# Kernel tuning notes

Measured on AMD Instinct MI355X. Metric: run time of the kernel, lower is better.

Reference implementation:

```python
import jax, jax.numpy as jnp
import numpy as np

B, SECL, WORDL = 16, 8, 512
S = SECL * WORDL
H, E, V, NOOV = 256, 128, 50000, 32
EOS = 3
FSIZE = 2  # config.mode == 'train'


def setup_inputs() -> dict:
    key = jax.random.key(0)
    ks = jax.random.split(key, 24)
    g = lambda i, shape, s=0.02: jax.random.normal(ks[i], shape, jnp.float32) * s
    inp = jax.random.randint(ks[0], (B,), 0, V)
    inp = inp.at[:4].set(EOS)  # exercise focus-update branch
    h = g(1, (B, H), 0.1)
    c = g(2, (B, H), 0.1)
    enc_outputs = g(3, (B, S, 2 * H), 1.0)
    enc_feature = g(4, (B, S, 2 * H), 0.1)
    enc_sec_output = g(5, (B, SECL, 2 * H), 1.0)
    enc_mask = jnp.ones((B, S), jnp.float32)
    sec_mask = jnp.ones((B, SECL), jnp.float32)
    prev_context = g(6, (B, 2 * H), 0.1)
    zeros_oov = jnp.zeros((B, NOOV), jnp.float32)
    enc_input_oov = jax.random.randint(ks[7], (B, S), 0, V + NOOV)
    coverage = jnp.zeros((B, S), jnp.float32)
    # sparse nonneg focus distribution over sections (guaranteed >=1 nonzero/row)
    u = jax.random.uniform(ks[8], (B, SECL))
    f = u * (u > 0.5)
    fb = jax.nn.one_hot(jnp.argmax(u, axis=1), SECL)
    f = jnp.where(f.sum(1, keepdims=True) > 0, f, fb)
    focus = f / f.sum(1, keepdims=True)
    params = dict(
        embedding=g(9, (V, E)),
        W_comb=g(10, (E, 2 * H + E)), b_comb=jnp.zeros((E,), jnp.float32),
        W_ih=g(11, (4 * H, E)), W_hh=g(12, (4 * H, H)),
        b_ih=jnp.zeros((4 * H,), jnp.float32), b_hh=jnp.zeros((4 * H,), jnp.float32),
        W_d=g(13, (2 * H, 2 * H)), b_d=jnp.zeros((2 * H,), jnp.float32),
        W_feat=g(14, (2 * H, 2 * H)), v_sec=g(15, (2 * H,)),
        W_dec=g(16, (2 * H, 2 * H)), b_dec=jnp.zeros((2 * H,), jnp.float32),
        w_cov=g(17, (2 * H,)), v_att=g(18, (2 * H,)),
        W_pgen=g(19, (1, 4 * H + E)), b_pgen=jnp.zeros((1,), jnp.float32),
        W_out=g(20, (V, 3 * H)), b_out=g(21, (V,)),
    )
    return dict(inp=inp, h=h, c=c, enc_outputs=enc_outputs, enc_feature=enc_feature,
                enc_sec_output=enc_sec_output, enc_mask=enc_mask, sec_mask=sec_mask,
                prev_context=prev_context, zeros_oov=zeros_oov, enc_input_oov=enc_input_oov,
                coverage=coverage, focus=focus, **params)


def _focus_update(focus, sad):
    # rem_mask: positions from the first nonzero of focus onward
    fz = jnp.cumprod((focus == 0).astype(sad.dtype), axis=1)
    rem_mask = (fz == 0).astype(sad.dtype)
    focus_index = jnp.sum(fz, axis=1).astype(jnp.int32)  # index of first nonzero
    focus_mask = jax.nn.one_hot(focus_index, SECL, dtype=sad.dtype)
    rem_ex = rem_mask - focus_mask
    focus_beta = sad * focus_mask
    rem_beta = sad * rem_ex
    max_rem_beta = rem_beta.max(axis=1)
    max_rem_ind = jnp.argmax(rem_beta, axis=1)
    compare = (focus_beta.max(axis=1) * 2 > max_rem_beta).astype(sad.dtype)[:, None]
    # train branch
    src = (max_rem_beta != 0).astype(sad.dtype)[:, None]
    max_rem_mask = jax.nn.one_hot(max_rem_ind, SECL, dtype=sad.dtype) * src
    cp2 = jnp.cumprod((max_rem_mask == 0).astype(sad.dtype), axis=1)
    after = (cp2 == 0).astype(sad.dtype) - max_rem_mask
    amb = sad * after
    mam_mask = (jax.nn.one_hot(jnp.argmax(amb, axis=1), SECL, dtype=sad.dtype)
                * (amb.max(axis=1) != 0).astype(sad.dtype)[:, None])
    case_f = focus_beta + sad * max_rem_mask
    case_r = sad * (max_rem_mask + mam_mask)
    fu = compare * case_f + (1 - compare) * case_r
    return fu / fu.sum(1, keepdims=True)


def reference(inp, h, c, enc_outputs, enc_feature, enc_sec_output, enc_mask, sec_mask,
              prev_context, zeros_oov, enc_input_oov, coverage, focus,
              embedding, W_comb, b_comb, W_ih, W_hh, b_ih, b_hh,
              W_d, b_d, W_feat, v_sec, W_dec, b_dec, w_cov, v_att,
              W_pgen, b_pgen, W_out, b_out):
    inp_is_eos = (inp == EOS).astype(jnp.float32)[:, None]  # [B,1] -> bcast over secL
    emb = embedding[inp]  # [B,E]
    x = jnp.concatenate([prev_context, emb], axis=1) @ W_comb.T + b_comb  # [B,E]
    # single LSTM step (torch gate order i,f,g,o)
    gates = x @ W_ih.T + b_ih + h @ W_hh.T + b_hh
    gi_, gf_, gg_, go_ = jnp.split(gates, 4, axis=1)
    c_new = jax.nn.sigmoid(gf_) * c + jax.nn.sigmoid(gi_) * jnp.tanh(gg_)
    h_new = jax.nn.sigmoid(go_) * jnp.tanh(c_new)
    dec_state = jnp.concatenate([h_new, c_new], axis=1)  # [B,2H]
    # section attention
    feat = enc_sec_output @ W_feat.T  # [B,secL,2H]
    d = dec_state @ W_d.T + b_d
    sc = jnp.tanh(feat + d[:, None, :]) @ v_sec  # [B,secL]
    sad = jax.nn.softmax(sc, axis=1) * sec_mask
    sad = sad / sad.sum(1, keepdims=True)
    # hard-attention focus update (only where input was EOS)
    fu = _focus_update(focus, sad)
    focus = inp_is_eos * fu + (1 - inp_is_eos) * focus
    # word attention with coverage
    dfeat = dec_state @ W_dec.T + b_dec
    att = enc_feature + dfeat[:, None, :] + coverage[:, :, None] * w_cov[None, None, :]
    score = jnp.tanh(att) @ v_att  # [B,S]
    score3 = score.reshape(B, SECL, WORDL)
    topk_focus, gidx = jax.lax.top_k(focus, FSIZE)  # [B,FSIZE]
    bidx = jnp.arange(B)[:, None]
    score_g = score3[bidx, gidx].reshape(B, FSIZE * WORDL)
    mask_g = enc_mask.reshape(B, SECL, WORDL)[bidx, gidx].reshape(B, FSIZE * WORDL)
    af = jax.nn.softmax(score_g, axis=1) * mask_g
    af = af / af.sum(1, keepdims=True)
    af = topk_focus[:, :, None] * af.reshape(B, FSIZE, WORDL)
    attn = jnp.zeros((B, SECL, WORDL), af.dtype).at[bidx, gidx].set(af).reshape(B, S)
    attn = attn / attn.sum(1, keepdims=True)
    context = jnp.einsum('bs,bsd->bd', attn, enc_outputs)  # [B,2H]
    coverage = coverage + attn
    # pointer-generator
    p_gen = jax.nn.sigmoid(jnp.concatenate([context, dec_state, x], axis=1) @ W_pgen.T + b_pgen)
    logits = jnp.concatenate([h_new, context], axis=1) @ W_out.T + b_out
    vocab_dist = jax.nn.softmax(logits, axis=1)
    vext = jnp.concatenate([p_gen * vocab_dist, zeros_oov], axis=1)  # [B,V+NOOV]
    final = vext.at[bidx, enc_input_oov].add((1 - p_gen) * attn)
    return final, h_new, c_new, context, attn, coverage, focus, sad
```

## Files before the change

kernel.cpp:

```cpp
#include <hip/hip_runtime.h>
#include <math.h>

#define NB 16
#define SECL 8
#define WORDL 512
#define SS 4096
#define HH 256
#define EE 128
#define VV 50000
#define NOOV 32
#define VO 50032
#define EOS_ID 3
#define H2 512
#define KOUT 768

#define OFF_FINAL 0
#define OFF_H    800512
#define OFF_C    804608
#define OFF_CTX  808704
#define OFF_ATTN 816896
#define OFF_COV  882432
#define OFF_FOC  947968
#define OFF_SAD  948096

#define WX     0
#define WD     2048
#define WDF    10240
#define WSC    18432
#define WGI    18560
#define WTF    18592
#define WSG    18624
#define WPART  35008
#define WPG    166080
#define WLG    166512

__device__ __forceinline__ float sigm(float x){ return 1.f/(1.f+__expf(-x)); }
__device__ __forceinline__ float tfast(float x){
  float ax = fabsf(x);
  float e  = __expf(-2.f*ax);
  float t  = (1.f-e)/(1.f+e);
  return x < 0.f ? -t : t;
}
__device__ __forceinline__ float dot4(float acc, float4 a, float4 b){
  acc = fmaf(a.x,b.x,acc); acc = fmaf(a.y,b.y,acc);
  acc = fmaf(a.z,b.z,acc); acc = fmaf(a.w,b.w,acc);
  return acc;
}
__device__ __forceinline__ float dot2(float acc, float2 a, float2 b){
  acc = fmaf(a.x,b.x,acc); acc = fmaf(a.y,b.y,acc);
  return acc;
}
__device__ __forceinline__ float mergep(float a, float b, int k, int lane){
  float send = (lane & k) ? a : b;
  float recv = __shfl_xor(send, k);
  return (lane & k) ? b + recv : a + recv;
}
__device__ __forceinline__ float reduce8(float acc[8], int lane){
  float m0 = mergep(acc[0], acc[1], 1, lane);
  float m1 = mergep(acc[2], acc[3], 1, lane);
  float m2 = mergep(acc[4], acc[5], 1, lane);
  float m3 = mergep(acc[6], acc[7], 1, lane);
  float n0 = mergep(m0, m1, 2, lane);
  float n1 = mergep(m2, m3, 2, lane);
  float p  = mergep(n0, n1, 4, lane);
  p += __shfl_xor(p, 8);
  p += __shfl_xor(p, 16);
  p += __shfl_xor(p, 32);
  return p;
}

__device__ __forceinline__ void focus_compute(int b, const float sc[SECL],
    const int* inp, const float* smask, const float* focus_in,
    float fo[SECL], float sad[SECL], int* pi1, int* pi2, float* pv1, float* pv2){
  float f[SECL];
  float mx = -1e30f;
  for(int l=0;l<SECL;l++) mx = fmaxf(mx, sc[l]);
  float sum = 0.f;
  for(int l=0;l<SECL;l++){ sad[l] = __expf(sc[l]-mx); sum += sad[l]; }
  float s2 = 0.f;
  for(int l=0;l<SECL;l++){ sad[l] = sad[l]/sum * smask[b*SECL+l]; s2 += sad[l]; }
  for(int l=0;l<SECL;l++) sad[l] /= s2;
  for(int l=0;l<SECL;l++) f[l] = focus_in[b*SECL+l];
  int fi = SECL;
  for(int l=0;l<SECL;l++){ if(f[l] != 0.f){ fi = l; break; } }
  float rem[SECL];
  for(int l=0;l<SECL;l++) rem[l] = (l > fi) ? sad[l] : 0.f;
  float mrb = rem[0]; int mri = 0;
  for(int l=1;l<SECL;l++){ if(rem[l] > mrb){ mrb = rem[l]; mri = l; } }
  float fbm = (fi < SECL) ? sad[fi] : 0.f;
  int cmp = (fbm*2.f > mrb);
  int src = (mrb != 0.f);
  float amb[SECL];
  for(int l=0;l<SECL;l++) amb[l] = (src && l > mri) ? sad[l] : 0.f;
  float am = amb[0]; int ai = 0;
  for(int l=1;l<SECL;l++){ if(amb[l] > am){ am = amb[l]; ai = l; } }
  float fu[SECL]; float fs = 0.f;
  for(int l=0;l<SECL;l++){
    float mrm = (src && l == mri) ? 1.f : 0.f;
    float mam = ((am != 0.f) && l == ai) ? 1.f : 0.f;
    float cf = ((l==fi) ? sad[l] : 0.f) + sad[l]*mrm;
    float cr = sad[l]*(mrm + mam);
    fu[l] = cmp ? cf : cr;
    fs += fu[l];
  }
  float eos = (inp[b] == EOS_ID) ? 1.f : 0.f;
  for(int l=0;l<SECL;l++)
    fo[l] = eos*(fu[l]/fs) + (1.f-eos)*f[l];
  float v1 = fo[0]; int i1 = 0;
  for(int l=1;l<SECL;l++){ if(fo[l] > v1){ v1 = fo[l]; i1 = l; } }
  float v2 = -1e30f; int i2 = 0;
  for(int l=0;l<SECL;l++){ if(l != i1 && fo[l] > v2){ v2 = fo[l]; i2 = l; } }
  *pi1 = i1; *pi2 = i2; *pv1 = v1; *pv2 = v2;
}


__global__ void __launch_bounds__(256)
k_x(const int* __restrict__ inp, const float* __restrict__ pc,
    const float* __restrict__ emb, const float* __restrict__ Wc,
    const float* __restrict__ bc, float* __restrict__ ws){
  int lane = threadIdx.x & 63;
  int gw = blockIdx.x*4 + (threadIdx.x >> 6);
  int bg = gw & 1, e = gw >> 1;
  float4 z = {0,0,0,0};
  float4 i0[8], i1[8], i2[8];
  #pragma unroll
  for(int j=0;j<8;j++){
    int b = bg*8 + j;
    i0[j] = *(const float4*)(pc + b*H2 + lane*4);
    i1[j] = *(const float4*)(pc + b*H2 + 256 + lane*4);
    i2[j] = (lane < 32) ? *(const float4*)(emb + (size_t)inp[b]*EE + lane*4) : z;
  }
  const float* wr = Wc + (size_t)e*(H2+EE);
  float4 w0 = *(const float4*)(wr + lane*4);
  float4 w1 = *(const float4*)(wr + 256 + lane*4);
  float4 w2 = (lane < 32) ? *(const float4*)(wr + 512 + lane*4) : z;
  float acc[8];
  #pragma unroll
  for(int j=0;j<8;j++){
    float a = dot4(0.f, w0, i0[j]);
    a = dot4(a, w1, i1[j]);
    a = dot4(a, w2, i2[j]);
    acc[j] = a;
  }
  float p = reduce8(acc, lane);
  if(lane < 8) ws[WX + (bg*8+lane)*EE + e] = p + bc[e];
}

__global__ void __launch_bounds__(256)
k_gates(const float* __restrict__ h, const float* __restrict__ c,
        const float* __restrict__ Wih, const float* __restrict__ Whh,
        const float* __restrict__ bih, const float* __restrict__ bhh,
        const float* __restrict__ ws, float* __restrict__ out){
  __shared__ float g_lds[4][8];
  int lane = threadIdx.x & 63;
  int wv   = threadIdx.x >> 6;
  int j  = blockIdx.x >> 1;
  int bg = blockIdx.x & 1;
  float2 xb[8]; float4 hb[8];
  #pragma unroll
  for(int q=0;q<8;q++){
    int b = bg*8 + q;
    xb[q] = *(const float2*)(ws + WX + b*EE + lane*2);
    hb[q] = *(const float4*)(h + b*HH + lane*4);
  }
  int r = wv*HH + j;
  float2 wx = *(const float2*)(Wih + (size_t)r*EE + lane*2);
  float4 wh = *(const float4*)(Whh + (size_t)r*HH + lane*4);
  float acc[8];
  #pragma unroll
  for(int q=0;q<8;q++)
    acc[q] = dot4(dot2(0.f, wx, xb[q]), wh, hb[q]);
  float p = reduce8(acc, lane);
  if(lane < 8) g_lds[wv][lane] = p + bih[r] + bhh[r];
  __syncthreads();
  if(threadIdx.x < 8){
    int b = bg*8 + threadIdx.x;
    float g0 = g_lds[0][threadIdx.x], g1 = g_lds[1][threadIdx.x];
    float g2 = g_lds[2][threadIdx.x], g3 = g_lds[3][threadIdx.x];
    float cn = sigm(g1)*c[b*HH + j] + sigm(g0)*tfast(g2);
    float hn = sigm(g3)*tfast(cn);
    out[OFF_H + b*HH + j] = hn;
    out[OFF_C + b*HH + j] = cn;
  }
}

__global__ void __launch_bounds__(256)
k_dd(const float* __restrict__ Wd, const float* __restrict__ bd,
     const float* __restrict__ Wdec, const float* __restrict__ bdec,
     const float* __restrict__ out, float* __restrict__ ws){
  int lane = threadIdx.x & 63;
  int gw = blockIdx.x*4 + (threadIdx.x >> 6);
  int bg = gw & 1, sel = (gw >> 1) & 1, j = gw >> 2;
  float4 d0[8], d1[8];
  #pragma unroll
  for(int q=0;q<8;q++){
    int b = bg*8 + q;
    d0[q] = *(const float4*)(out + OFF_H + b*HH + lane*4);
    d1[q] = *(const float4*)(out + OFF_C + b*HH + lane*4);
  }
  const float* wr = (sel ? Wdec : Wd) + (size_t)j*H2;
  float4 w0 = *(const float4*)(wr + lane*4);
  float4 w1 = *(const float4*)(wr + 256 + lane*4);
  float acc[8];
  #pragma unroll
  for(int q=0;q<8;q++)
    acc[q] = dot4(dot4(0.f, w0, d0[q]), w1, d1[q]);
  float p = reduce8(acc, lane);
  if(lane < 8) ws[(sel ? WDF : WD) + (bg*8+lane)*H2 + j] = p + (sel ? bdec : bd)[j];
}

__global__ void __launch_bounds__(256)
k_sec(const float* __restrict__ eso, const float* __restrict__ Wf,
      const float* __restrict__ vsec, float* __restrict__ ws){
  __shared__ float red[4];
  int lane = threadIdx.x & 63;
  int wv   = threadIdx.x >> 6;
  int bl = blockIdx.x; int b = bl >> 3;
  const float* ep = eso + (size_t)bl*H2;
  float4 es0 = *(const float4*)(ep + lane*4);
  float4 es1 = *(const float4*)(ep + 256 + lane*4);
  const float* dp = ws + WD + b*H2;
  float local = 0.f;
  for(int t=0;t<16;t++){
    int j0 = wv*8 + t*32;
    float acc[8];
    #pragma unroll
    for(int jj=0;jj<8;jj++){
      const float* wr = Wf + (size_t)(j0+jj)*H2;
      float4 w0 = *(const float4*)(wr + lane*4);
      float4 w1 = *(const float4*)(wr + 256 + lane*4);
      acc[jj] = dot4(dot4(0.f, w0, es0), w1, es1);
    }
    float p = reduce8(acc, lane);
    if(lane < 8){
      int j = j0 + lane;
      local += tfast(p + dp[j]) * vsec[j];
    }
  }
  local += __shfl_xor(local, 1);
  local += __shfl_xor(local, 2);
  local += __shfl_xor(local, 4);
  if(lane == 0) red[wv] = local;
  __syncthreads();
  if(threadIdx.x == 0) ws[WSC + bl] = red[0]+red[1]+red[2]+red[3];
}

__global__ void __launch_bounds__(256)
k_score(const float* __restrict__ ef, const float* __restrict__ cov,
        const float* __restrict__ wcov, const float* __restrict__ vatt,
        const int* __restrict__ inp, const float* __restrict__ smask,
        const float* __restrict__ foc,
        float* __restrict__ ws, float* __restrict__ out){
  __shared__ int   gi_l[NB*2];
  __shared__ float tf_l[NB*2];
  int tid = threadIdx.x;
  if(tid < NB){
    int b = tid;
    float sc[SECL];
    for(int l=0;l<SECL;l++) sc[l] = ws[WSC + b*SECL + l];
    float fo[SECL], sad[SECL]; int i1,i2; float v1,v2;
    focus_compute(b, sc, inp, smask, foc, fo, sad, &i1, &i2, &v1, &v2);
    gi_l[b*2] = i1; gi_l[b*2+1] = i2;
    tf_l[b*2] = v1; tf_l[b*2+1] = v2;
    if(blockIdx.x == 0){
      for(int l=0;l<SECL;l++){
        out[OFF_SAD + b*SECL + l] = sad[l];
        out[OFF_FOC + b*SECL + l] = fo[l];
      }
      ((int*)ws)[WGI + b*2]     = i1;
      ((int*)ws)[WGI + b*2 + 1] = i2;
      ws[WTF + b*2]     = v1;
      ws[WTF + b*2 + 1] = v2;
    }
  }
  __syncthreads();
  int lane = tid & 63;
  int o = blockIdx.x*4 + (tid >> 6);
  int b = o >> 10, fidx = (o >> 9) & 1, w = o & 511;
  int g = gi_l[b*2 + fidx];
  int s = g*WORDL + w;
  const float* e  = ef + ((size_t)(b*SS + s))*H2;
  const float* df = ws + WDF + b*H2;
  float cv = cov[b*SS + s];
  int j = lane*4;
  float local = 0.f;
  #pragma unroll
  for(int half=0; half<2; half++){
    int jj = j + half*256;
    float4 a  = *(const float4*)(e+jj);
    float4 d4 = *(const float4*)(df+jj);
    float4 wc = *(const float4*)(wcov+jj);
    float4 va = *(const float4*)(vatt+jj);
    local += tfast(a.x + d4.x + cv*wc.x)*va.x;
    local += tfast(a.y + d4.y + cv*wc.y)*va.y;
    local += tfast(a.z + d4.z + cv*wc.z)*va.z;
    local += tfast(a.w + d4.w + cv*wc.w)*va.w;
  }
  for(int off=32; off>0; off>>=1) local += __shfl_xor(local, off);
  if(lane == 0) ws[WSG + o] = local;
}

__global__ void k_af(const float* __restrict__ emask, const float* __restrict__ cov,
                     float* __restrict__ ws, float* __restrict__ out){
  __shared__ float es[1024];
  __shared__ float red[256];
  int b = blockIdx.x, tid = threadIdx.x;
  int g0 = ((int*)ws)[WGI+b*2], g1 = ((int*)ws)[WGI+b*2+1];
  float tf0 = ws[WTF+b*2], tf1 = ws[WTF+b*2+1];
  float lm = -1e30f;
  for(int i=tid;i<1024;i+=256) lm = fmaxf(lm, ws[WSG + b*1024 + i]);
  red[tid] = lm; __syncthreads();
  for(int off=128; off; off>>=1){
    if(tid < off) red[tid] = fmaxf(red[tid], red[tid+off]);
    __syncthreads();
  }
  float mx = red[0]; __syncthreads();
  float ls0 = 0.f, ls1 = 0.f;
  for(int i=tid;i<1024;i+=256){
    int fidx = i >> 9, w = i & 511;
    int g = fidx ? g1 : g0;
    float m = emask[b*SS + g*WORDL + w];
    float ev = __expf(ws[WSG + b*1024 + i] - mx)*m;
    es[i] = ev;
    if(fidx) ls1 += ev; else ls0 += ev;
  }
  red[tid] = ls0; __syncthreads();
  for(int off=128; off; off>>=1){ if(tid<off) red[tid]+=red[tid+off]; __syncthreads(); }
  float sum0 = red[0]; __syncthreads();
  red[tid] = ls1; __syncthreads();
  for(int off=128; off; off>>=1){ if(tid<off) red[tid]+=red[tid+off]; __syncthreads(); }
  float sum1 = red[0]; __syncthreads();
  float inv = 1.f/(tf0*sum0 + tf1*sum1);
  for(int s=tid;s<SS;s+=256){
    int sec = s >> 9, w = s & 511;
    float a = 0.f;
    if(sec == g0)      a = tf0*es[w]*inv;
    else if(sec == g1) a = tf1*es[512+w]*inv;
    out[OFF_ATTN + b*SS + s] = a;
    out[OFF_COV  + b*SS + s] = cov[b*SS+s] + a;
  }
}

__global__ void k_ctxp(const float* __restrict__ eo, const float* __restrict__ out,
                       float* __restrict__ ws){
  int blk = blockIdx.x; int b = blk >> 4, ch = blk & 15;
  int d = threadIdx.x;
  int g0 = ((const int*)ws)[WGI + b*2];
  int g1 = ((const int*)ws)[WGI + b*2 + 1];
  float a0 = 0.f, a1 = 0.f;
  #pragma unroll 4
  for(int p = ch*64; p < ch*64 + 64; p++){
    int s = ((p >> 9) ? g1 : g0)*WORDL + (p & 511);
    float a = out[OFF_ATTN + b*SS + s];
    const float* ep = eo + ((size_t)(b*SS + s))*H2;
    a0 = fmaf(a, ep[d],       a0);
    a1 = fmaf(a, ep[d+256],   a1);
  }
  ws[WPART + (size_t)blk*H2 + d]       = a0;
  ws[WPART + (size_t)blk*H2 + d + 256] = a1;
}

__global__ void k_ctx(const float* __restrict__ Wp, const float* __restrict__ bp,
                      float* __restrict__ ws, float* __restrict__ out){
  __shared__ float red[256];
  int b = blockIdx.x, tid = threadIdx.x;
  float c0 = 0.f, c1 = 0.f;
  for(int ch=0; ch<16; ch++){
    c0 += ws[WPART + (size_t)(b*16+ch)*H2 + tid];
    c1 += ws[WPART + (size_t)(b*16+ch)*H2 + tid + 256];
  }
  out[OFF_CTX + b*H2 + tid]       = c0;
  out[OFF_CTX + b*H2 + tid + 256] = c1;
  float hn = out[OFF_H + b*HH + tid];
  float cn = out[OFF_C + b*HH + tid];
  float pv = c0*Wp[tid] + c1*Wp[tid+256] + hn*Wp[512+tid] + cn*Wp[768+tid];
  if(tid < EE) pv = fmaf(ws[WX + b*EE + tid], Wp[1024+tid], pv);
  red[tid] = pv; __syncthreads();
  for(int off=128; off; off>>=1){ if(tid<off) red[tid]+=red[tid+off]; __syncthreads(); }
  if(tid == 0) ws[WPG + b] = sigm(red[0] + bp[0]);
}

#define LG_NBLK 768
#define LG_ROWS 16
#define LG_WIN  (LG_NBLK*LG_ROWS)
#define LG_NWIN 5
__global__ void __launch_bounds__(256,3)
k_logits(const float* __restrict__ Wout, const float* __restrict__ bout,
         const float* __restrict__ out, float* __restrict__ ws){
  int lane = threadIdx.x & 63;
  int wv   = threadIdx.x >> 6;
  int bg   = wv & 1;
  int rh   = wv >> 1;
  float4 hb0[8], hb1[8], hb2[8];
  #pragma unroll
  for(int j=0;j<8;j++){
    int b = bg*8 + j;
    hb0[j] = *(const float4*)(out + OFF_H   + b*HH + lane*4);
    hb1[j] = *(const float4*)(out + OFF_CTX + b*H2 + lane*4);
    hb2[j] = *(const float4*)(out + OFF_CTX + b*H2 + 256 + lane*4);
  }
  for(int w=0; w<LG_NWIN; w++){
    int v0 = w*LG_WIN + blockIdx.x*LG_ROWS + rh*8;
    if(v0 >= VV) break;
    int va = v0;
    const float* pa = Wout + (size_t)va*KOUT + lane*4;
    float4 A0 = *(const float4*)(pa);
    float4 A1 = *(const float4*)(pa+256);
    float4 A2 = *(const float4*)(pa+512);
    int vb = v0+1; int vbc = vb < VV ? vb : VV-1;
    const float* pb = Wout + (size_t)vbc*KOUT + lane*4;
    float4 B0 = *(const float4*)(pb);
    float4 B1 = *(const float4*)(pb+256);
    float4 B2 = *(const float4*)(pb+512);
    #pragma unroll
    for(int r=0;r<8;r++){
      int v = v0 + r;
      float4 C0=B0, C1=B1, C2=B2;
      if(r < 6){
        int vn = v0 + r + 2; int vnc = vn < VV ? vn : VV-1;
        const float* np = Wout + (size_t)vnc*KOUT + lane*4;
        C0 = *(const float4*)(np);
        C1 = *(const float4*)(np+256);
        C2 = *(const float4*)(np+512);
      }
      float acc[8];
      #pragma unroll
      for(int q=0;q<8;q++){
        float a = dot4(0.f, A0, hb0[q]);
        a = dot4(a, A1, hb1[q]);
        a = dot4(a, A2, hb2[q]);
        acc[q] = a;
      }
      float p = reduce8(acc, lane);
      if(v < VV && lane < 8)
        ws[WLG + (size_t)(bg*8+lane)*VV + v] = p + bout[v];
      A0=B0; A1=B1; A2=B2;
      B0=C0; B1=C1; B2=C2;
    }
  }
}

__global__ void __launch_bounds__(1024)
k_out(const float* __restrict__ zoov, const int* __restrict__ oov,
      float* __restrict__ ws, float* __restrict__ out){
  __shared__ float rm[1024], rs[1024];
  int b = blockIdx.x, tid = threadIdx.x;
  float mt = -1e30f, st = 0.f;
  for(int v=tid; v<VV; v+=1024){
    float x = ws[WLG + (size_t)b*VV + v];
    if(x > mt){ st = st*__expf(mt - x) + 1.f; mt = x; }
    else       st += __expf(x - mt);
  }
  rm[tid] = mt; rs[tid] = st; __syncthreads();
  for(int off=512; off; off>>=1){
    if(tid < off){
      float ma = rm[tid], mb = rm[tid+off];
      float M = fmaxf(ma, mb);
      rs[tid] = rs[tid]*__expf(ma-M) + rs[tid+off]*__expf(mb-M);
      rm[tid] = M;
    }
    __syncthreads();
  }
  float mx = rm[0], sm = rs[0];
  float pg = ws[WPG + b];
  float scale = pg / sm;
  for(int v=tid; v<VO; v+=1024){
    float r = (v < VV) ? scale*__expf(ws[WLG + (size_t)b*VV + v] - mx)
                       : zoov[b*NOOV + v - VV];
    out[OFF_FINAL + (size_t)b*VO + v] = r;
  }
  __syncthreads();
  int fidx = tid >> 9, w = tid & 511;
  int g = ((const int*)ws)[WGI + b*2 + fidx];
  int s = g*WORDL + w;
  float a = out[OFF_ATTN + b*SS + s];
  if(a != 0.f)
    atomicAdd(out + OFF_FINAL + (size_t)b*VO + oov[b*SS + s], (1.f - pg)*a);
}

extern "C" void kernel_launch(void* const* d_in, const int* in_sizes, int n_in,
                              void* d_out, int out_size, void* d_ws, size_t ws_size,
                              hipStream_t stream){
  const int*   inp   = (const int*)  d_in[0];
  const float* h     = (const float*)d_in[1];
  const float* c     = (const float*)d_in[2];
  const float* eo    = (const float*)d_in[3];
  const float* efeat = (const float*)d_in[4];
  const float* eso   = (const float*)d_in[5];
  const float* emask = (const float*)d_in[6];
  const float* smask = (const float*)d_in[7];
  const float* pctx  = (const float*)d_in[8];
  const float* zoov  = (const float*)d_in[9];
  const int*   oov   = (const int*)  d_in[10];
  const float* cov   = (const float*)d_in[11];
  const float* foc   = (const float*)d_in[12];
  const float* emb   = (const float*)d_in[13];
  const float* Wc    = (const float*)d_in[14];
  const float* bc    = (const float*)d_in[15];
  const float* Wih   = (const float*)d_in[16];
  const float* Whh   = (const float*)d_in[17];
  const float* bih   = (const float*)d_in[18];
  const float* bhh   = (const float*)d_in[19];
  const float* Wd    = (const float*)d_in[20];
  const float* bd    = (const float*)d_in[21];
  const float* Wf    = (const float*)d_in[22];
  const float* vsec  = (const float*)d_in[23];
  const float* Wdec  = (const float*)d_in[24];
  const float* bdec  = (const float*)d_in[25];
  const float* wcov  = (const float*)d_in[26];
  const float* vatt  = (const float*)d_in[27];
  const float* Wp    = (const float*)d_in[28];
  const float* bp    = (const float*)d_in[29];
  const float* Wout  = (const float*)d_in[30];
  const float* bout  = (const float*)d_in[31];
  float* out = (float*)d_out;
  float* ws  = (float*)d_ws;

  k_x      <<<64,      256,  0, stream>>>(inp, pctx, emb, Wc, bc, ws);
  k_gates  <<<512,     256,  0, stream>>>(h, c, Wih, Whh, bih, bhh, ws, out);
  k_dd     <<<512,     256,  0, stream>>>(Wd, bd, Wdec, bdec, out, ws);
  k_sec    <<<128,     256,  0, stream>>>(eso, Wf, vsec, ws);
  k_score  <<<4096,    256,  0, stream>>>(efeat, cov, wcov, vatt, inp, smask, foc, ws, out);
  k_af     <<<16,      256,  0, stream>>>(emask, cov, ws, out);
  k_ctxp   <<<256,     256,  0, stream>>>(eo, out, ws);
  k_ctx    <<<16,      256,  0, stream>>>(Wp, bp, ws, out);
  k_logits <<<LG_NBLK, 256,  0, stream>>>(Wout, bout, out, ws);
  k_out    <<<16,      1024, 0, stream>>>(zoov, oov, ws, out);
}
```

Measured before the change: 153.7 us.

## Stride vocab rows across blocks in logits kernel with continuous prefetch pipeline

Changes the W_out row assignment in the logits kernel. Each block previously handled contiguous runs of 16 rows inside 5 windows, restarting the prefetch pipeline at every window. Now each wave walks rows with a grid-wide stride over 33 iterations, keeping the two-ahead prefetch running without restarts. At any moment all blocks read adjacent rows, which changes DRAM access locality and removes the per-window pipeline warm-up.

```diff
diff --git a/kernel.cpp b/kernel.cpp
--- a/kernel.cpp
+++ b/kernel.cpp
@@ -380,10 +380,9 @@
   if(tid == 0) ws[WPG + b] = sigm(red[0] + bp[0]);
 }
 
-#define LG_NBLK 768
-#define LG_ROWS 16
-#define LG_WIN  (LG_NBLK*LG_ROWS)
-#define LG_NWIN 5
+#define LG_NBLK  768
+#define LG_STRIDE (LG_NBLK*2)
+#define LG_ITERS 33
 __global__ void __launch_bounds__(256,3)
 k_logits(const float* __restrict__ Wout, const float* __restrict__ bout,
          const float* __restrict__ out, float* __restrict__ ws){
@@ -399,44 +398,39 @@
     hb1[j] = *(const float4*)(out + OFF_CTX + b*H2 + lane*4);
     hb2[j] = *(const float4*)(out + OFF_CTX + b*H2 + 256 + lane*4);
   }
-  for(int w=0; w<LG_NWIN; w++){
-    int v0 = w*LG_WIN + blockIdx.x*LG_ROWS + rh*8;
-    if(v0 >= VV) break;
-    int va = v0;
-    const float* pa = Wout + (size_t)va*KOUT + lane*4;
-    float4 A0 = *(const float4*)(pa);
-    float4 A1 = *(const float4*)(pa+256);
-    float4 A2 = *(const float4*)(pa+512);
-    int vb = v0+1; int vbc = vb < VV ? vb : VV-1;
-    const float* pb = Wout + (size_t)vbc*KOUT + lane*4;
-    float4 B0 = *(const float4*)(pb);
-    float4 B1 = *(const float4*)(pb+256);
-    float4 B2 = *(const float4*)(pb+512);
+  int vbase = blockIdx.x*2 + rh;
+  const float* p0 = Wout + (size_t)vbase*KOUT + lane*4;
+  float4 A0 = *(const float4*)(p0);
+  float4 A1 = *(const float4*)(p0+256);
+  float4 A2 = *(const float4*)(p0+512);
+  int v1c = vbase + LG_STRIDE; if(v1c >= VV) v1c = VV-1;
+  const float* p1 = Wout + (size_t)v1c*KOUT + lane*4;
+  float4 B0 = *(const float4*)(p1);
+  float4 B1 = *(const float4*)(p1+256);
+  float4 B2 = *(const float4*)(p1+512);
+  for(int j=0;j<LG_ITERS;j++){
+    int v = vbase + j*LG_STRIDE;
+    float4 C0=B0, C1=B1, C2=B2;
+    if(j < LG_ITERS-2){
+      int vn = v + 2*LG_STRIDE; if(vn >= VV) vn = VV-1;
+      const float* np = Wout + (size_t)vn*KOUT + lane*4;
+      C0 = *(const float4*)(np);
+      C1 = *(const float4*)(np+256);
+      C2 = *(const float4*)(np+512);
+    }
+    float acc[8];
     #pragma unroll
-    for(int r=0;r<8;r++){
-      int v = v0 + r;
-      float4 C0=B0, C1=B1, C2=B2;
-      if(r < 6){
-        int vn = v0 + r + 2; int vnc = vn < VV ? vn : VV-1;
-        const float* np = Wout + (size_t)vnc*KOUT + lane*4;
-        C0 = *(const float4*)(np);
-        C1 = *(const float4*)(np+256);
-        C2 = *(const float4*)(np+512);
-      }
-      float acc[8];
-      #pragma unroll
-      for(int q=0;q<8;q++){
-        float a = dot4(0.f, A0, hb0[q]);
-        a = dot4(a, A1, hb1[q]);
-        a = dot4(a, A2, hb2[q]);
-        acc[q] = a;
-      }
-      float p = reduce8(acc, lane);
-      if(v < VV && lane < 8)
-        ws[WLG + (size_t)(bg*8+lane)*VV + v] = p + bout[v];
-      A0=B0; A1=B1; A2=B2;
-      B0=C0; B1=C1; B2=C2;
+    for(int q=0;q<8;q++){
+      float a = dot4(0.f, A0, hb0[q]);
+      a = dot4(a, A1, hb1[q]);
+      a = dot4(a, A2, hb2[q]);
+      acc[q] = a;
     }
+    float p = reduce8(acc, lane);
+    if(v < VV && lane < 8)
+      ws[WLG + (size_t)(bg*8+lane)*VV + v] = p + bout[v];
+    A0=B0; A1=B1; A2=B2;
+    B0=C0; B1=C1; B2=C2;
   }
 }
 
```

Measured after the change: 163.1 us. +6.1%, slower.
